# Kernel optimization log

Hardware: AMD Instinct MI355X
Metric: run time of the kernel (lower is better)

Reference implementation:

```python
import jax, jax.numpy as jnp
import numpy as np

D_MODEL, D_QKV, N_HEADS = 1024, 64, 16


def setup_inputs() -> dict:
    key = jax.random.key(0)
    k_x, k_qkv, k_out = jax.random.split(key, 3)
    X = jax.random.normal(k_x, (2, 2048, D_MODEL), dtype=jnp.float32)
    # nn.Linear(d_model, 3*d_qkv*n_heads, bias=False): store as (in, out) for X @ W
    W_qkv = jax.random.normal(k_qkv, (D_MODEL, 3 * D_QKV * N_HEADS), dtype=jnp.float32) * (D_MODEL ** -0.5)
    W_out = jax.random.normal(k_out, (D_QKV * N_HEADS, D_MODEL), dtype=jnp.float32) * ((D_QKV * N_HEADS) ** -0.5)
    return {"X": X, "W_qkv": W_qkv, "W_out": W_out}


def reference(X, W_qkv, W_out):
    b, s, _ = X.shape
    h, d = N_HEADS, D_QKV
    scale = d ** 0.5
    qkv = X @ W_qkv                          # [b, s, 3*h*d]
    # Faithful to torch: view(b, s, h, d, 3).unbind(-1) -> interleaved q/k/v layout
    qkv = qkv.reshape(b, s, h, d, 3)
    q, k, v = qkv[..., 0], qkv[..., 1], qkv[..., 2]   # each [b, s, h, d]
    scores = jnp.einsum("bqhd,bkhd->bhqk", q, k) / scale
    weights = jax.nn.softmax(scores, axis=-1)          # [b, h, s, s]
    attn = jnp.einsum("bhqk,bkhd->bqhd", weights, v)   # [b, s, h, d]
    return attn.reshape(b, s, h * d) @ W_out           # [b, s, d_model]
```

## Files before the change

kernel.cpp:

```cpp
#include <hip/hip_runtime.h>
#include <hip/hip_bf16.h>
#include <math.h>

typedef __bf16 bf16;
typedef __bf16 bf16x2 __attribute__((ext_vector_type(2)));
typedef __bf16 bf16x4 __attribute__((ext_vector_type(4)));
typedef __bf16 bf16x8 __attribute__((ext_vector_type(8)));
typedef float f32x4 __attribute__((ext_vector_type(4)));
typedef float f32x16 __attribute__((ext_vector_type(16)));
typedef int i32x2 __attribute__((ext_vector_type(2)));
typedef int i32x4 __attribute__((ext_vector_type(4)));

#define MFMA16(a, b, c) __builtin_amdgcn_mfma_f32_16x16x32_bf16(a, b, c, 0, 0, 0)
#define MFMA32(a, b, c) __builtin_amdgcn_mfma_f32_32x32x16_bf16(a, b, c, 0, 0, 0)

constexpr int D_MODEL = 1024;
constexpr int N_QKV   = 3072;
constexpr int BATCH   = 2;
constexpr int SEQ     = 2048;
constexpr int NH      = 16;
constexpr int DH      = 64;
constexpr int M_TOT   = BATCH * SEQ;

__device__ __forceinline__ void gl_lds16(const bf16* g, bf16* l) {
    __builtin_amdgcn_global_load_lds(
        (const __attribute__((address_space(1))) void*)g,
        (__attribute__((address_space(3))) void*)l, 16, 0, 0);
}

__device__ __forceinline__ void pl32swap(int& a, int& b) {
    i32x2 r = __builtin_amdgcn_permlane32_swap(a, b, false, false);
    a = r[0];
    b = r[1];
}

template <int N> __device__ __forceinline__ void waitv() {
    asm volatile("s_waitcnt vmcnt(%0)" :: "n"(N) : "memory");
}
__device__ __forceinline__ void waitlgkm0() {
    asm volatile("s_waitcnt lgkmcnt(0)" ::: "memory");
}

__device__ __forceinline__ void transpose_tile(
    const float* __restrict__ in, bf16* __restrict__ out,
    int K, int N, int n0, int k0, bf16 (*T)[72], bool permute)
{
    const int tid = threadIdx.x;
    const int r   = tid >> 2;
    const int c4  = (tid & 3) * 16;

    const float* src = in + (size_t)(k0 + r) * N + n0 + c4;
    f32x4 v0 = *(const f32x4*)(src + 0);
    f32x4 v1 = *(const f32x4*)(src + 4);
    f32x4 v2 = *(const f32x4*)(src + 8);
    f32x4 v3 = *(const f32x4*)(src + 12);
    #pragma unroll
    for (int j = 0; j < 4; j++) {
        T[c4 + j][r]      = (bf16)v0[j];
        T[c4 + 4 + j][r]  = (bf16)v1[j];
        T[c4 + 8 + j][r]  = (bf16)v2[j];
        T[c4 + 12 + j][r] = (bf16)v3[j];
    }
    __syncthreads();
    int rowg = n0 + r;
    if (permute) {
        const int which = rowg % 3;
        const int h     = rowg / 192;
        const int d     = (rowg % 192) / 3;
        rowg = which * 1024 + h * 64 + d;
    }
    bf16* dst = out + (size_t)rowg * K + k0 + c4;
    *(bf16x8*)(dst)     = *(const bf16x8*)&T[r][c4];
    *(bf16x8*)(dst + 8) = *(const bf16x8*)&T[r][c4 + 8];
}

__global__ __launch_bounds__(256) void prepass_kernel(
    const float* __restrict__ X, const float* __restrict__ Wqkv,
    const float* __restrict__ Wout,
    bf16* __restrict__ xb, bf16* __restrict__ wqkv_t, bf16* __restrict__ wout_t)
{
    __shared__ bf16 T[64][72];
    const int b = blockIdx.x;
    if (b < 2048) {
        const size_t i = ((size_t)b * 256 + threadIdx.x) * 8;
        f32x4 a0 = *(const f32x4*)(X + i);
        f32x4 a1 = *(const f32x4*)(X + i + 4);
        bf16x8 w;
        #pragma unroll
        for (int j = 0; j < 4; j++) { w[j] = (bf16)a0[j]; w[j + 4] = (bf16)a1[j]; }
        *(bf16x8*)(xb + i) = w;
    } else if (b < 2048 + 768) {
        const int idx = b - 2048;
        transpose_tile(Wqkv, wqkv_t, D_MODEL, N_QKV,
                       (idx % 48) * 64, (idx / 48) * 64, T, true);
    } else {
        const int idx = b - 2816;
        transpose_tile(Wout, wout_t, D_MODEL, D_MODEL,
                       (idx % 16) * 64, (idx / 16) * 64, T, false);
    }
}

__global__ __launch_bounds__(512, 2) void qkv_gemm_kernel(
    const bf16* __restrict__ Xb, const bf16* __restrict__ Wt,
    bf16* __restrict__ qb, bf16* __restrict__ kb, bf16* __restrict__ vb)
{
    __shared__ __align__(16) bf16 smem[65536];
    bf16* const sA = smem;
    bf16* const sB = smem + 32768;

    const int tid  = threadIdx.x;
    const int wave = tid >> 6;
    const int lane = tid & 63;
    const int quad = lane >> 4;
    const int l16  = lane & 15;
    const int wr   = wave >> 2;
    const int wc   = wave & 3;
    const int m0   = blockIdx.x * 256;
    const int n0   = blockIdx.y * 256;

    const int sr2  = tid >> 3;
    const int c8p  = (tid & 7) ^ (sr2 & 7);
    const int stR0 = (sr2 << 1) | (c8p >> 2);
    const int stC0 = (c8p & 3) << 3;

    const bf16* Asrc = Xb + (size_t)(m0 + stR0) * D_MODEL + stC0;
    const bf16* Bsrc = Wt + (size_t)(n0 + stR0) * D_MODEL + stC0;

#define STG(s, kbo)                                                          \
    do {                                                                     \
        gl_lds16(Asrc + (kbo),                 sA + (s) * 8192 + tid * 8);   \
        gl_lds16(Asrc + 128 * D_MODEL + (kbo), sA + (s) * 8192 + 4096 + tid * 8); \
        gl_lds16(Bsrc + (kbo),                 sB + (s) * 8192 + tid * 8);   \
        gl_lds16(Bsrc + 128 * D_MODEL + (kbo), sB + (s) * 8192 + 4096 + tid * 8); \
    } while (0)

    const int foff = ((l16 >> 1) << 6) +
                     (((((l16 & 1) << 2) | quad) ^ ((l16 >> 1) & 7)) << 3);

    f32x4 acc[8][4];
    #pragma unroll
    for (int a = 0; a < 8; a++)
        #pragma unroll
        for (int b = 0; b < 4; b++) acc[a][b] = {0.f, 0.f, 0.f, 0.f};

#define PHASE(s, jn, DOSTG, WV)                                              \
    {                                                                        \
        const bf16* Ab_ = sA + (s) * 8192 + wr * 4096;                       \
        const bf16* Bb_ = sB + (s) * 8192 + wc * 2048;                       \
        bf16x8 af[8], bfr[4];                                                \
        _Pragma("unroll") for (int mi = 0; mi < 8; mi++)                     \
            af[mi] = *(const bf16x8*)&Ab_[mi * 512 + foff];                  \
        _Pragma("unroll") for (int ni = 0; ni < 4; ni++)                     \
            bfr[ni] = *(const bf16x8*)&Bb_[ni * 512 + foff];                 \
        waitlgkm0();                                                         \
        __builtin_amdgcn_s_barrier();                                        \
        if (DOSTG) { STG((s), (jn) * 32); }                                  \
        __builtin_amdgcn_s_setprio(1);                                       \
        _Pragma("unroll") for (int mi = 0; mi < 8; mi++)                     \
            _Pragma("unroll") for (int ni = 0; ni < 4; ni++)                 \
                acc[mi][ni] = MFMA16(af[mi], bfr[ni], acc[mi][ni]);          \
        __builtin_amdgcn_s_setprio(0);                                       \
        waitv<WV>();                                                         \
        __builtin_amdgcn_s_barrier();                                        \
    }

    STG(0, 0); STG(1, 32); STG(2, 64); STG(3, 96);
    waitv<12>();
    __builtin_amdgcn_s_barrier();

    for (int t = 0; t < 7; ++t) {
        const int j = t * 4;
        PHASE(0, j + 4, true, 12)
        PHASE(1, j + 5, true, 12)
        PHASE(2, j + 6, true, 12)
        PHASE(3, j + 7, true, 12)
    }
    PHASE(0, 0, false, 8)
    PHASE(1, 0, false, 4)
    PHASE(2, 0, false, 0)
    PHASE(3, 0, false, 0)

#undef PHASE
#undef STG

    const int bb     = m0 >> 11;
    const int s_base = m0 & (SEQ - 1);

    if (n0 < 2048) {
        bf16* dst0 = (n0 < 1024) ? qb : kb;
        const int h = ((n0 + wc * 64) >> 6) & 15;
        const size_t bh = (size_t)(bb * NH + h);
        #pragma unroll
        for (int mi = 0; mi < 8; mi++) {
            const int s0 = s_base + wr * 128 + mi * 16 + quad * 4;
            #pragma unroll
            for (int ni = 0; ni < 4; ni++) {
                const int d = ni * 16 + l16;
                #pragma unroll
                for (int i = 0; i < 4; i++)
                    dst0[(bh * SEQ + s0 + i) * DH + d] = (bf16)acc[mi][ni][i];
            }
        }
    } else {
        __syncthreads();
        bf16* T = smem;
        #pragma unroll
        for (int ni = 0; ni < 4; ni++) {
            const int nl = wc * 64 + ni * 16 + l16;
            #pragma unroll
            for (int mi = 0; mi < 8; mi++) {
                const int ml = wr * 128 + mi * 16 + quad * 4;
                bf16x4 pv;
                #pragma unroll
                for (int i = 0; i < 4; i++) pv[i] = (bf16)acc[mi][ni][i];
                const int c   = ml >> 3;
                const int swz = (c & 24) | ((c ^ nl) & 7);
                *(bf16x4*)&T[nl * 256 + swz * 8 + (ml & 7)] = pv;
            }
        }
        __syncthreads();
        const int hbase = (n0 - 2048) >> 6;
        #pragma unroll
        for (int it = 0; it < 8; it++) {
            const int nl = (tid >> 4) + it * 32;
            const int h  = hbase + (nl >> 6);
            const int d  = nl & 63;
            const size_t obase = ((size_t)(bb * NH + h) * DH + d) * SEQ + s_base;
            #pragma unroll
            for (int cc = 0; cc < 2; cc++) {
                const int c   = (tid & 15) + cc * 16;
                const int swz = (c & 24) | ((c ^ nl) & 7);
                bf16x8 vv = *(const bf16x8*)&T[nl * 256 + swz * 8];
                *(bf16x8*)(vb + obase + c * 8) = vv;
            }
        }
    }
}

__global__ __launch_bounds__(512, 4) void attn_kernel(
    const bf16* __restrict__ qb, const bf16* __restrict__ kb,
    const bf16* __restrict__ vb, bf16* __restrict__ ob)
{
    __shared__ __align__(16) bf16 smem[32768];

    const int tid  = threadIdx.x;
    const int wave = tid >> 6;
    const int grp  = wave >> 2;
    const int wq   = wave & 3;
    const int lane = tid & 63;
    const int l32  = lane & 31;
    const int hi   = lane >> 5;
    const int ltid = tid & 255;
    const int bh   = blockIdx.x;
    const int q0   = blockIdx.y * 128;
    const size_t base  = (size_t)bh * SEQ * DH;
    const int    kbase = grp * (SEQ / 2);

    bf16* const KsB = smem + grp * 2 * 4096;
    bf16* const VtB = smem + 16384 + grp * 2 * 4096;

    constexpr float QSCALE = 0.125f * 1.44269504f;

    bf16x8 qf[4];
    {
        const size_t qoff = base + (size_t)(q0 + wq * 32 + l32) * DH + hi * 8;
        #pragma unroll
        for (int kc = 0; kc < 4; kc++) {
            qf[kc] = *(const bf16x8*)(qb + qoff + kc * 16);
            #pragma unroll
            for (int j = 0; j < 8; j++)
                qf[kc][j] = (bf16)((float)qf[kc][j] * QSCALE);
        }
    }

    bf16x8 ones;
    #pragma unroll
    for (int j = 0; j < 8; j++) ones[j] = (bf16)1.0f;

    f32x16 o_acc[2];
    f32x16 o_l;
    #pragma unroll
    for (int i = 0; i < 16; i++) {
        o_acc[0][i] = 0.f; o_acc[1][i] = 0.f; o_l[i] = 0.f;
    }

    const int so0 = ltid;
    const int so1 = 256 + ltid;
    const int sr0 = so0 >> 3, sc0 = ((so0 & 7) ^ (sr0 & 7)) * 8;
    const int sr1 = so1 >> 3, sc1 = ((so1 & 7) ^ (sr1 & 7)) * 8;

    #define STAGE(bufi, kk0)                                                   \
        do {                                                                   \
            gl_lds16(kb + base + (size_t)(kbase + (kk0) + sr0) * DH + sc0,     \
                     KsB + (bufi) * 4096 + so0 * 8);                           \
            gl_lds16(kb + base + (size_t)(kbase + (kk0) + sr1) * DH + sc1,     \
                     KsB + (bufi) * 4096 + so1 * 8);                           \
            gl_lds16(vb + base + (size_t)sr0 * SEQ + kbase + (kk0) + sc0,      \
                     VtB + (bufi) * 4096 + so0 * 8);                           \
            gl_lds16(vb + base + (size_t)sr1 * SEQ + kbase + (kk0) + sc1,      \
                     VtB + (bufi) * 4096 + so1 * 8);                           \
        } while (0)

    STAGE(0, 0);
    int buf = 0;

    for (int kt = 0; kt < SEQ / 128; ++kt) {
        __syncthreads();
        if (kt + 1 < SEQ / 128) STAGE(buf ^ 1, (kt + 1) * 64);

        const bf16* Kst = KsB + buf * 4096;
        const bf16* Vtt = VtB + buf * 4096;

        #pragma unroll
        for (int kblk = 0; kblk < 2; kblk++) {
            f32x16 sacc;
            #pragma unroll
            for (int i = 0; i < 16; i++) sacc[i] = 0.f;
            #pragma unroll
            for (int kc = 0; kc < 4; kc++) {
                const int cko = ((2 * kc + hi) ^ (l32 & 7)) * 8;
                bf16x8 kf = *(const bf16x8*)
                    &Kst[(kblk * 32 + l32) * 64 + cko];
                sacc = MFMA32(kf, qf[kc], sacc);
            }

            int w[8];
            #pragma unroll
            for (int c = 0; c < 8; c++) {
                bf16x2 t;
                t[0] = (bf16)__builtin_amdgcn_exp2f(sacc[2 * c]);
                t[1] = (bf16)__builtin_amdgcn_exp2f(sacc[2 * c + 1]);
                w[c] = __builtin_bit_cast(int, t);
            }
            #pragma unroll
            for (int cc = 0; cc < 2; cc++) {
                pl32swap(w[cc * 4 + 0], w[cc * 4 + 2]);
                pl32swap(w[cc * 4 + 1], w[cc * 4 + 3]);
                i32x4 fi = {w[cc * 4 + 0], w[cc * 4 + 1],
                            w[cc * 4 + 2], w[cc * 4 + 3]};
                bf16x8 pa = __builtin_bit_cast(bf16x8, fi);

                const int kc = kblk * 2 + cc;
                const int cko = ((2 * kc + hi) ^ (l32 & 7)) * 8;
                o_l = MFMA32(pa, ones, o_l);
                #pragma unroll
                for (int nb = 0; nb < 2; nb++) {
                    bf16x8 vf = *(const bf16x8*)
                        &Vtt[(nb * 32 + l32) * 64 + cko];
                    o_acc[nb] = MFMA32(pa, vf, o_acc[nb]);
                }
            }
        }
        buf ^= 1;
    }
    #undef STAGE

    float* cO  = (float*)smem;
    float* cL1 = (float*)smem + 8192;

    __syncthreads();
    if (grp == 1) {
        #pragma unroll
        for (int nb = 0; nb < 2; nb++)
            #pragma unroll
            for (int c4 = 0; c4 < 4; c4++) {
                const int j = nb * 4 + c4;
                f32x4 v = { o_acc[nb][c4 * 4 + 0], o_acc[nb][c4 * 4 + 1],
                            o_acc[nb][c4 * 4 + 2], o_acc[nb][c4 * 4 + 3] };
                *(f32x4*)&cO[(wq * 64 + lane) * 32 + ((j ^ (lane & 7)) * 4)] = v;
            }
        if (l32 == 0) {
            #pragma unroll
            for (int i = 0; i < 16; i++)
                cL1[wq * 32 + ((i & 3) + 8 * (i >> 2) + 4 * hi)] = o_l[i];
        }
    }
    __syncthreads();
    if (grp == 0) {
        #pragma unroll
        for (int nb = 0; nb < 2; nb++)
            #pragma unroll
            for (int c4 = 0; c4 < 4; c4++) {
                const int j = nb * 4 + c4;
                f32x4 v = *(const f32x4*)
                    &cO[(wq * 64 + lane) * 32 + ((j ^ (lane & 7)) * 4)];
                #pragma unroll
                for (int e = 0; e < 4; e++) o_acc[nb][c4 * 4 + e] += v[e];
            }
        const int b = bh >> 4, h = bh & 15;
        #pragma unroll
        for (int i = 0; i < 16; i++) {
            const int qrow = (i & 3) + 8 * (i >> 2) + 4 * hi;
            const int q = q0 + wq * 32 + qrow;
            const float li = 1.0f / (o_l[i] + cL1[wq * 32 + qrow]);
            #pragma unroll
            for (int nb = 0; nb < 2; nb++)
                ob[((size_t)(b * SEQ + q) * NH + h) * DH + nb * 32 + l32] =
                    (bf16)(o_acc[nb][i] * li);
        }
    }
}

__global__ __launch_bounds__(256, 2) void out_gemm_kernel(
    const bf16* __restrict__ A, const bf16* __restrict__ Wt,
    float* __restrict__ out)
{
    __shared__ __align__(16) bf16 smem[32768];
    bf16* const sA = smem;
    bf16* const sB = smem + 16384;

    const int tid  = threadIdx.x;
    const int wave = tid >> 6;
    const int lane = tid & 63;
    const int quad = lane >> 4;
    const int l16  = lane & 15;
    const int wr   = wave >> 1;
    const int wc   = wave & 1;
    const int m0   = blockIdx.x * 128;
    const int n0   = blockIdx.y * 128;

    const int sr2  = tid >> 3;
    const int c8p  = (tid & 7) ^ (sr2 & 7);
    const int stR0 = (sr2 << 1) | (c8p >> 2);
    const int stC0 = (c8p & 3) << 3;

    const bf16* Asrc = A  + (size_t)(m0 + stR0) * D_MODEL + stC0;
    const bf16* Bsrc = Wt + (size_t)(n0 + stR0) * D_MODEL + stC0;

#define STG(s, kbo)                                                          \
    do {                                                                     \
        gl_lds16(Asrc + (kbo),                sA + (s) * 4096 + tid * 8);    \
        gl_lds16(Asrc + 64 * D_MODEL + (kbo), sA + (s) * 4096 + 2048 + tid * 8); \
        gl_lds16(Bsrc + (kbo),                sB + (s) * 4096 + tid * 8);    \
        gl_lds16(Bsrc + 64 * D_MODEL + (kbo), sB + (s) * 4096 + 2048 + tid * 8); \
    } while (0)

    const int foff = ((l16 >> 1) << 6) +
                     (((((l16 & 1) << 2) | quad) ^ ((l16 >> 1) & 7)) << 3);

    f32x4 acc[4][4];
    #pragma unroll
    for (int a = 0; a < 4; a++)
        #pragma unroll
        for (int b = 0; b < 4; b++) acc[a][b] = {0.f, 0.f, 0.f, 0.f};

#define PHASE(s, jn, DOSTG, WV)                                              \
    {                                                                        \
        const bf16* Ab_ = sA + (s) * 4096 + wr * 2048;                       \
        const bf16* Bb_ = sB + (s) * 4096 + wc * 2048;                       \
        bf16x8 af[4], bfr[4];                                                \
        _Pragma("unroll") for (int mi = 0; mi < 4; mi++)                     \
            af[mi] = *(const bf16x8*)&Ab_[mi * 512 + foff];                  \
        _Pragma("unroll") for (int ni = 0; ni < 4; ni++)                     \
            bfr[ni] = *(const bf16x8*)&Bb_[ni * 512 + foff];                 \
        waitlgkm0();                                                         \
        __builtin_amdgcn_s_barrier();                                        \
        if (DOSTG) { STG((s), (jn) * 32); }                                  \
        __builtin_amdgcn_s_setprio(1);                                       \
        _Pragma("unroll") for (int mi = 0; mi < 4; mi++)                     \
            _Pragma("unroll") for (int ni = 0; ni < 4; ni++)                 \
                acc[mi][ni] = MFMA16(af[mi], bfr[ni], acc[mi][ni]);          \
        __builtin_amdgcn_s_setprio(0);                                       \
        waitv<WV>();                                                         \
        __builtin_amdgcn_s_barrier();                                        \
    }

    STG(0, 0); STG(1, 32); STG(2, 64); STG(3, 96);
    waitv<12>();
    __builtin_amdgcn_s_barrier();

    for (int t = 0; t < 7; ++t) {
        const int j = t * 4;
        PHASE(0, j + 4, true, 12)
        PHASE(1, j + 5, true, 12)
        PHASE(2, j + 6, true, 12)
        PHASE(3, j + 7, true, 12)
    }
    PHASE(0, 0, false, 8)
    PHASE(1, 0, false, 4)
    PHASE(2, 0, false, 0)
    PHASE(3, 0, false, 0)

#undef PHASE
#undef STG

    #pragma unroll
    for (int mi = 0; mi < 4; mi++) {
        const int row0 = m0 + wr * 64 + mi * 16 + quad * 4;
        #pragma unroll
        for (int ni = 0; ni < 4; ni++) {
            const int n = n0 + wc * 64 + ni * 16 + l16;
            #pragma unroll
            for (int i = 0; i < 4; i++)
                out[(size_t)(row0 + i) * D_MODEL + n] = acc[mi][ni][i];
        }
    }
}

extern "C" void kernel_launch(void* const* d_in, const int* in_sizes, int n_in,
                              void* d_out, int out_size, void* d_ws, size_t ws_size,
                              hipStream_t stream)
{
    const float* X    = (const float*)d_in[0];
    const float* Wqkv = (const float*)d_in[1];
    const float* Wout = (const float*)d_in[2];
    float* out        = (float*)d_out;

    const size_t n_elem = (size_t)M_TOT * D_MODEL;
    bf16* qb      = (bf16*)d_ws;
    bf16* kb      = qb + n_elem;
    bf16* vb      = kb + n_elem;
    bf16* attnb   = vb + n_elem;
    bf16* wqkv_t  = attnb + n_elem;
    bf16* wout_t  = wqkv_t + (size_t)N_QKV * D_MODEL;
    bf16* xb      = wout_t + (size_t)D_MODEL * D_MODEL;

    prepass_kernel<<<3072, 256, 0, stream>>>(X, Wqkv, Wout, xb, wqkv_t, wout_t);

    qkv_gemm_kernel<<<dim3(M_TOT / 256, N_QKV / 256), 512, 0, stream>>>(
        xb, wqkv_t, qb, kb, vb);
    attn_kernel<<<dim3(BATCH * NH, SEQ / 128), 512, 0, stream>>>(qb, kb, vb, attnb);
    out_gemm_kernel<<<dim3(M_TOT / 128, D_MODEL / 128), 256, 0, stream>>>(
        attnb, wout_t, out);
}
```

Measured before the change: 170.2 us.

## Double-buffer QKV GEMM register fragments and compute softmax row sums with VALU

The QKV projection GEMM now keeps two register sets of A/B fragments, loading the next stage's fragments from LDS between MFMA groups. This removes the per-phase LDS-read wait before compute, and the pipeline depth drops from four staged tiles to three in flight. In attention, the row-sum MFMA against a ones vector is replaced by scalar float accumulation of the fp32 exponentials plus a cross-lane shuffle, with an extra LDS round trip and barrier to combine the sums. The row sums now come from unrounded fp32 values rather than bf16, and register pressure rises in the GEMM.

```diff
diff --git a/kernel.cpp b/kernel.cpp
--- a/kernel.cpp
+++ b/kernel.cpp
@@ -143,42 +143,59 @@
         #pragma unroll
         for (int b = 0; b < 4; b++) acc[a][b] = {0.f, 0.f, 0.f, 0.f};
 
-#define PHASE(s, jn, DOSTG, WV)                                              \
+    bf16x8 afA[8], bfA[4], afB[8], bfB[4];
+
+    STG(0, 0); STG(1, 32); STG(2, 64);
+    waitv<4>();
+    __builtin_amdgcn_s_barrier();
+    {
+        const bf16* A0 = sA + wr * 4096;
+        const bf16* B0 = sB + wc * 2048;
+        #pragma unroll
+        for (int mi = 0; mi < 8; mi++)
+            afA[mi] = *(const bf16x8*)&A0[mi * 512 + foff];
+        #pragma unroll
+        for (int ni = 0; ni < 4; ni++)
+            bfA[ni] = *(const bf16x8*)&B0[ni * 512 + foff];
+    }
+
+    int p = 0;
+
+#define PHASE(CA, CB, NA, NB, DOSTG, DONXT, WV)                              \
     {                                                                        \
-        const bf16* Ab_ = sA + (s) * 8192 + wr * 4096;                       \
-        const bf16* Bb_ = sB + (s) * 8192 + wc * 2048;                       \
-        bf16x8 af[8], bfr[4];                                                \
-        _Pragma("unroll") for (int mi = 0; mi < 8; mi++)                     \
-            af[mi] = *(const bf16x8*)&Ab_[mi * 512 + foff];                  \
-        _Pragma("unroll") for (int ni = 0; ni < 4; ni++)                     \
-            bfr[ni] = *(const bf16x8*)&Bb_[ni * 512 + foff];                 \
-        waitlgkm0();                                                         \
-        __builtin_amdgcn_s_barrier();                                        \
-        if (DOSTG) { STG((s), (jn) * 32); }                                  \
+        if (DOSTG) { const int kst = p + 3; STG((kst & 3), kst * 32); }      \
+        const int sn = (p + 1) & 3;                                          \
+        const bf16* An_ = sA + sn * 8192 + wr * 4096;                        \
+        const bf16* Bn_ = sB + sn * 8192 + wc * 2048;                        \
         __builtin_amdgcn_s_setprio(1);                                       \
-        _Pragma("unroll") for (int mi = 0; mi < 8; mi++)                     \
+        _Pragma("unroll") for (int c = 0; c < 4; c++) {                      \
+            _Pragma("unroll") for (int m2 = 0; m2 < 2; m2++)                 \
+                _Pragma("unroll") for (int ni = 0; ni < 4; ni++)             \
+                    acc[c * 2 + m2][ni] =                                    \
+                        MFMA16(CA[c * 2 + m2], CB[ni], acc[c * 2 + m2][ni]); \
+            if (DONXT) {                                                     \
+                NA[c * 2]     = *(const bf16x8*)&An_[(c * 2) * 512 + foff];  \
+                NA[c * 2 + 1] = *(const bf16x8*)&An_[(c * 2 + 1) * 512 + foff]; \
+            }                                                                \
+        }                                                                    \
+        if (DONXT) {                                                         \
             _Pragma("unroll") for (int ni = 0; ni < 4; ni++)                 \
-                acc[mi][ni] = MFMA16(af[mi], bfr[ni], acc[mi][ni]);          \
+                NB[ni] = *(const bf16x8*)&Bn_[ni * 512 + foff];              \
+        }                                                                    \
         __builtin_amdgcn_s_setprio(0);                                       \
         waitv<WV>();                                                         \
         __builtin_amdgcn_s_barrier();                                        \
-    }
-
-    STG(0, 0); STG(1, 32); STG(2, 64); STG(3, 96);
-    waitv<12>();
-    __builtin_amdgcn_s_barrier();
-
-    for (int t = 0; t < 7; ++t) {
-        const int j = t * 4;
-        PHASE(0, j + 4, true, 12)
-        PHASE(1, j + 5, true, 12)
-        PHASE(2, j + 6, true, 12)
-        PHASE(3, j + 7, true, 12)
-    }
-    PHASE(0, 0, false, 8)
-    PHASE(1, 0, false, 4)
-    PHASE(2, 0, false, 0)
-    PHASE(3, 0, false, 0)
+        ++p;                                                                 \
+    }
+
+    for (int t = 0; t < 14; ++t) {
+        PHASE(afA, bfA, afB, bfB, true, true, 4)
+        PHASE(afB, bfB, afA, bfA, true, true, 4)
+    }
+    PHASE(afA, bfA, afB, bfB, true,  true,  4)
+    PHASE(afB, bfB, afA, bfA, false, true,  0)
+    PHASE(afA, bfA, afB, bfB, false, true,  0)
+    PHASE(afB, bfB, afA, bfA, false, false, 0)
 
 #undef PHASE
 #undef STG
@@ -273,16 +290,10 @@
         }
     }
 
-    bf16x8 ones;
+    f32x16 o_acc[2];
     #pragma unroll
-    for (int j = 0; j < 8; j++) ones[j] = (bf16)1.0f;
-
-    f32x16 o_acc[2];
-    f32x16 o_l;
-    #pragma unroll
-    for (int i = 0; i < 16; i++) {
-        o_acc[0][i] = 0.f; o_acc[1][i] = 0.f; o_l[i] = 0.f;
-    }
+    for (int i = 0; i < 16; i++) { o_acc[0][i] = 0.f; o_acc[1][i] = 0.f; }
+    float l_acc = 0.f;
 
     const int so0 = ltid;
     const int so1 = 256 + ltid;
@@ -327,9 +338,11 @@
             int w[8];
             #pragma unroll
             for (int c = 0; c < 8; c++) {
-                bf16x2 t;
-                t[0] = (bf16)__builtin_amdgcn_exp2f(sacc[2 * c]);
-                t[1] = (bf16)__builtin_amdgcn_exp2f(sacc[2 * c + 1]);
+                const float e0 = __builtin_amdgcn_exp2f(sacc[2 * c]);
+                const float e1 = __builtin_amdgcn_exp2f(sacc[2 * c + 1]);
+                l_acc += e0;
+                l_acc += e1;
+                bf16x2 t; t[0] = (bf16)e0; t[1] = (bf16)e1;
                 w[c] = __builtin_bit_cast(int, t);
             }
             #pragma unroll
@@ -342,7 +355,6 @@
 
                 const int kc = kblk * 2 + cc;
                 const int cko = ((2 * kc + hi) ^ (l32 & 7)) * 8;
-                o_l = MFMA32(pa, ones, o_l);
                 #pragma unroll
                 for (int nb = 0; nb < 2; nb++) {
                     bf16x8 vf = *(const bf16x8*)
@@ -355,8 +367,11 @@
     }
     #undef STAGE
 
+    const float l_q = l_acc + __shfl_xor(l_acc, 32);
+
     float* cO  = (float*)smem;
     float* cL1 = (float*)smem + 8192;
+    float* cL2 = (float*)smem + 8320;
 
     __syncthreads();
     if (grp == 1) {
@@ -369,11 +384,7 @@
                             o_acc[nb][c4 * 4 + 2], o_acc[nb][c4 * 4 + 3] };
                 *(f32x4*)&cO[(wq * 64 + lane) * 32 + ((j ^ (lane & 7)) * 4)] = v;
             }
-        if (l32 == 0) {
-            #pragma unroll
-            for (int i = 0; i < 16; i++)
-                cL1[wq * 32 + ((i & 3) + 8 * (i >> 2) + 4 * hi)] = o_l[i];
-        }
+        if (hi == 0) cL1[wq * 32 + l32] = l_q;
     }
     __syncthreads();
     if (grp == 0) {
@@ -387,12 +398,16 @@
                 #pragma unroll
                 for (int e = 0; e < 4; e++) o_acc[nb][c4 * 4 + e] += v[e];
             }
+        if (hi == 0) cL2[wq * 32 + l32] = l_q + cL1[wq * 32 + l32];
+    }
+    __syncthreads();
+    if (grp == 0) {
         const int b = bh >> 4, h = bh & 15;
         #pragma unroll
         for (int i = 0; i < 16; i++) {
             const int qrow = (i & 3) + 8 * (i >> 2) + 4 * hi;
             const int q = q0 + wq * 32 + qrow;
-            const float li = 1.0f / (o_l[i] + cL1[wq * 32 + qrow]);
+            const float li = 1.0f / cL2[wq * 32 + qrow];
             #pragma unroll
             for (int nb = 0; nb < 2; nb++)
                 ob[((size_t)(b * SEQ + q) * NH + h) * DH + nb * 32 + l32] =
```

Result: faster. 162.0 us (-4.8%).
